# Kernel tuning notes

Hardware: AMD Instinct MI355X
Metric: run time of the kernel (lower is better)

The kernel has to match this reference:

```python
import jax, jax.numpy as jnp
import numpy as np

B, M, N = 2, 256, 256
K, P, Q, D = 8, 512, 512, 64
R, Pp, Qp, Dp = 128, 512, 512, 64
TEMP = float(np.sqrt(Dp))  # softmax temperature = sqrt(D')


def _xavier(key, shape):
    # xavier_uniform over last two dims (fan_in, fan_out), matching torch init on (K, d, D)
    fan_in, fan_out = shape[-2], shape[-1]
    lim = float(np.sqrt(6.0 / (fan_in + fan_out)))
    return jax.random.uniform(key, shape, jnp.float32, -lim, lim)


def setup_inputs() -> dict:
    key = jax.random.key(0)
    ks = jax.random.split(key, 9)
    return {
        "z": jax.random.normal(ks[0], (B, M, N, R), jnp.float32),
        "y_q": jax.random.normal(ks[1], (B, N, Qp), jnp.float32),
        "x_k": jax.random.normal(ks[2], (B, M, Pp), jnp.float32),
        "Theta_x": _xavier(ks[3], (K, P, D)),
        "Theta_y": _xavier(ks[4], (K, Q, D)),
        "Lam_x": _xavier(ks[5], (K, Pp, Dp)),
        "Lam_y": _xavier(ks[6], (K, Qp, Dp)),
        "Lam_zx": _xavier(ks[7], (K, R, Dp)),
        "Lam_zy": _xavier(ks[8], (K, R, Dp)),
    }


def reference(z, y_q, x_k, Theta_x, Theta_y, Lam_x, Lam_y, Lam_zx, Lam_zy):
    # --- mixed attention scores ---
    xt = jnp.einsum('bmp,kpd->bkmd', x_k, Lam_x)          # [B,K,M,D']
    yt = jnp.einsum('bnq,kqd->bknd', y_q, Lam_y)          # [B,K,N,D']
    r = jnp.einsum('bkmd,bknd->bkmn', xt, yt)             # pairwise term
    zy = jnp.einsum('bmnr,krd->bkmnd', z, Lam_zy)         # [B,K,M,N,D'] (large)
    r = r + jnp.einsum('bkmnd,bkmd->bkmn', zy, xt)
    r = r + jnp.einsum('bknd,bmnr,krd->bkmn', yt, z, Lam_zx)
    # --- generalised convolution (mask=None, bias=False) ---
    a = jax.nn.softmax(r / TEMP, axis=-2)                 # softmax over M (column-wise)
    xv = jnp.einsum('bmp,kpd->bkmd', x_k, Theta_x)        # value projection
    y = jnp.einsum('bkmn,bkmd,kqd->bnq', a, xv, Theta_y)  # [B,N,Q]
    return y
```

## Files before the change

kernel.cpp:

```cpp
#include <hip/hip_runtime.h>
#include <hip/hip_bf16.h>

#define LOG2E_OVER_T 0.18033688011112042f

typedef __attribute__((ext_vector_type(8))) short short8;
typedef __attribute__((ext_vector_type(4))) float f32x4;
typedef unsigned short ushort_t;
typedef unsigned long long ull_t;

#define MFMA16(a, b, c) __builtin_amdgcn_mfma_f32_16x16x32_bf16(a, b, c, 0, 0, 0)

__device__ __forceinline__ ushort_t f2bf(float f) {
    union { float f; unsigned u; } v; v.f = f;
    unsigned r = (v.u + 0x7fffu + ((v.u >> 16) & 1u)) >> 16;
    return (ushort_t)r;
}

__device__ __forceinline__ void split8(const float4 a, const float4 b,
                                       short8& hi, short8& lo)
{
    union { float f[8]; unsigned u[8]; } Z;
    Z.f[0] = a.x; Z.f[1] = a.y; Z.f[2] = a.z; Z.f[3] = a.w;
    Z.f[4] = b.x; Z.f[5] = b.y; Z.f[6] = b.z; Z.f[7] = b.w;
    union { unsigned u[4]; short8 s; } H, L;
    #pragma unroll
    for (int i = 0; i < 4; i++) {
        const unsigned u0 = Z.u[2 * i], u1 = Z.u[2 * i + 1];
        H.u[i] = __builtin_amdgcn_perm(u1, u0, 0x07060302u);
        union { unsigned u; float f; } h0, h1;
        h0.u = u0 & 0xffff0000u; h1.u = u1 & 0xffff0000u;
        union { float f; unsigned u; } l0, l1;
        l0.f = Z.f[2 * i] - h0.f; l1.f = Z.f[2 * i + 1] - h1.f;
        L.u[i] = __builtin_amdgcn_perm(l1.u, l0.u, 0x07060302u);
    }
    hi = H.s; lo = L.s;
}

__device__ __forceinline__ void mfma_core64(
    const ushort_t* __restrict__ Ag, int lda,
    const ushort_t* __restrict__ Btg, int ldb,
    int ksteps, f32x4 acc[2][2])
{
    __shared__ __align__(16) ushort_t As[64 * 40];
    __shared__ __align__(16) ushort_t Bs[64 * 40];
    const int t = threadIdx.x;
    const int srow = t >> 2, skc = (t & 3) * 8;
    const int lane = t & 63, w = t >> 6;
    const int wr = w >> 1, wc = w & 1;
    const int fr = lane & 15, kg = lane >> 4;
    const int aoff = (wr * 32 + fr) * 40 + kg * 8;
    const int boff = (wc * 32 + fr) * 40 + kg * 8;
    const long arow = (long)srow * lda + skc;
    const long brow = (long)srow * ldb + skc;

    short8 ra = *(const short8*)(Ag + arow);
    short8 rb = *(const short8*)(Btg + brow);
    for (int kt = 0; kt < ksteps; kt++) {
        __syncthreads();
        *(short8*)&As[srow * 40 + skc] = ra;
        *(short8*)&Bs[srow * 40 + skc] = rb;
        __syncthreads();
        if (kt + 1 < ksteps) {
            ra = *(const short8*)(Ag + arow + (kt + 1) * 32);
            rb = *(const short8*)(Btg + brow + (kt + 1) * 32);
        }
        short8 a0 = *(const short8*)&As[aoff];
        short8 a1 = *(const short8*)&As[aoff + 16 * 40];
        short8 b0 = *(const short8*)&Bs[boff];
        short8 b1 = *(const short8*)&Bs[boff + 16 * 40];
        acc[0][0] = MFMA16(a0, b0, acc[0][0]);
        acc[0][1] = MFMA16(a0, b1, acc[0][1]);
        acc[1][0] = MFMA16(a1, b0, acc[1][0]);
        acc[1][1] = MFMA16(a1, b1, acc[1][1]);
    }
}

__device__ __forceinline__ void zero_acc(f32x4 acc[2][2]) {
    const f32x4 z4 = {0.f, 0.f, 0.f, 0.f};
    acc[0][0] = z4; acc[0][1] = z4; acc[1][0] = z4; acc[1][1] = z4;
}

__global__ __launch_bounds__(256)
void convert_kernel(const float* __restrict__ x_k, const float* __restrict__ y_q,
                    const float* __restrict__ Lam_x, const float* __restrict__ Theta_x,
                    const float* __restrict__ Lam_y, const float* __restrict__ Lam_zy,
                    const float* __restrict__ Lam_zx, const float* __restrict__ Theta_y,
                    ushort_t* __restrict__ xkb, ushort_t* __restrict__ yqb,
                    ushort_t* __restrict__ WxTb, ushort_t* __restrict__ WyTb,
                    ushort_t* __restrict__ Zyb, ushort_t* __restrict__ Zxb,
                    ushort_t* __restrict__ TyTb, float* __restrict__ ssum)
{
    int i = blockIdx.x * 256 + threadIdx.x;
    if (i < 262144) { xkb[i] = f2bf(x_k[i]); return; }
    i -= 262144;
    if (i < 262144) { yqb[i] = f2bf(y_q[i]); return; }
    i -= 262144;
    if (i < 524288) {
        const int k = i >> 16, rem = i & 65535, dc = rem >> 9, p = i & 511;
        const float v = (dc < 64) ? Lam_x[((long)k * 512 + p) * 64 + dc]
                                  : Theta_x[((long)k * 512 + p) * 64 + dc - 64];
        WxTb[i] = f2bf(v); return;
    }
    i -= 524288;
    if (i < 262144) {
        const int k = i >> 15, d = (i >> 9) & 63, p = i & 511;
        WyTb[i] = f2bf(Lam_y[((long)k * 512 + p) * 64 + d]); return;
    }
    i -= 262144;
    if (i < 65536) { Zyb[i] = f2bf(Lam_zy[i]); return; }
    i -= 65536;
    if (i < 65536) { Zxb[i] = f2bf(Lam_zx[i]); return; }
    i -= 65536;
    if (i < 262144) {
        const int q = i >> 9, kd = i & 511, k = kd >> 6, d = kd & 63;
        TyTb[i] = f2bf(Theta_y[((long)k * 512 + q) * 64 + d]); return;
    }
    i -= 262144;
    ssum[i] = 0.f;
}

__global__ __launch_bounds__(256)
void proj_kernel(const ushort_t* __restrict__ xkb, const ushort_t* __restrict__ yqb,
                 const ushort_t* __restrict__ WxTb, const ushort_t* __restrict__ WyTb,
                 ushort_t* __restrict__ xtb, ushort_t* __restrict__ ytb,
                 ushort_t* __restrict__ xvTb)
{
    const int side = blockIdx.z;
    const int bx = blockIdx.x, by = blockIdx.y;
    if (side == 1 && bx >= 8) return;
    f32x4 acc[2][2]; zero_acc(acc);
    const int t = threadIdx.x, lane = t & 63, w = t >> 6;
    const int wr = w >> 1, wc = w & 1, fr = lane & 15, kg = lane >> 4;

    if (side == 0) {
        mfma_core64(xkb + (long)(by * 64) * 512, 512,
                    WxTb + (long)(bx * 64) * 512, 512, 16, acc);
        const int k = bx >> 1, isxv = bx & 1;
        #pragma unroll
        for (int mi = 0; mi < 2; mi++)
        #pragma unroll
        for (int ni = 0; ni < 2; ni++) {
            const int grow0 = by * 64 + wr * 32 + mi * 16 + kg * 4;
            const int b = grow0 >> 8, m0 = grow0 & 255;
            const int d = wc * 32 + ni * 16 + fr;
            if (!isxv) {
                #pragma unroll
                for (int j = 0; j < 4; j++)
                    xtb[(((long)(b * 8 + k)) * 256 + m0 + j) * 64 + d] = f2bf(acc[mi][ni][j]);
            } else {
                ull_t pk = (ull_t)f2bf(acc[mi][ni][0])
                         | ((ull_t)f2bf(acc[mi][ni][1]) << 16)
                         | ((ull_t)f2bf(acc[mi][ni][2]) << 32)
                         | ((ull_t)f2bf(acc[mi][ni][3]) << 48);
                *(ull_t*)&xvTb[(((long)(b * 8 + k)) * 64 + d) * 256 + m0] = pk;
            }
        }
    } else {
        mfma_core64(yqb + (long)(by * 64) * 512, 512,
                    WyTb + (long)(bx * 64) * 512, 512, 16, acc);
        const int k = bx;
        #pragma unroll
        for (int mi = 0; mi < 2; mi++)
        #pragma unroll
        for (int ni = 0; ni < 2; ni++)
        #pragma unroll
        for (int j = 0; j < 4; j++) {
            const int grow = by * 64 + wr * 32 + mi * 16 + kg * 4 + j;
            const int b = grow >> 8, n = grow & 255;
            const int d = wc * 32 + ni * 16 + fr;
            ytb[(((long)(b * 8 + k)) * 256 + n) * 64 + d] = f2bf(acc[mi][ni][j]);
        }
    }
}

__global__ __launch_bounds__(256)
void step2_kernel(const ushort_t* __restrict__ xtb, const ushort_t* __restrict__ ytb,
                  const ushort_t* __restrict__ Zyb, const ushort_t* __restrict__ Zxb,
                  ushort_t* __restrict__ wzyb, ushort_t* __restrict__ wzxb)
{
    const int bz = blockIdx.x;
    const int which = bz >> 7, idx = bz & 127;
    const int bk = idx >> 3, tile = idx & 7, mt = tile >> 1, nt = tile & 1;
    const int k = bk & 7;
    const ushort_t* Ag  = (which ? ytb : xtb) + ((long)bk * 256 + mt * 64) * 64;
    const ushort_t* Btg = (which ? Zxb : Zyb) + ((long)k * 128 + nt * 64) * 64;
    ushort_t* C = which ? wzxb : wzyb;
    const long coff = ((long)bk * 256 + mt * 64) * 128 + nt * 64;
    f32x4 acc[2][2]; zero_acc(acc);
    mfma_core64(Ag, 64, Btg, 64, 2, acc);
    const int t = threadIdx.x, lane = t & 63, w = t >> 6;
    const int wr = w >> 1, wc = w & 1, fr = lane & 15, kg = lane >> 4;
    #pragma unroll
    for (int mi = 0; mi < 2; mi++)
    #pragma unroll
    for (int ni = 0; ni < 2; ni++)
    #pragma unroll
    for (int j = 0; j < 4; j++)
        C[coff + (long)(wr * 32 + mi * 16 + kg * 4 + j) * 128 + wc * 32 + ni * 16 + fr]
            = f2bf(acc[mi][ni][j]);
}

__global__ __launch_bounds__(256, 4)
void fused_score(const float* __restrict__ z,
                 const ushort_t* __restrict__ xtb, const ushort_t* __restrict__ ytb,
                 const ushort_t* __restrict__ wzyb, const ushort_t* __restrict__ wzxb,
                 ushort_t* __restrict__ Et, float* __restrict__ ssum)
{
    const int nt = blockIdx.x, mt = blockIdx.y, b = blockIdx.z;
    const int m0 = mt * 8, n0 = nt * 16;
    __shared__ float sc[8 * 8 * 17];
    const int t = threadIdx.x, lane = t & 63, w = t >> 6;
    const int fr = lane & 15, kg = lane >> 4;
    const int f8 = fr & 7;

    {
        const long ybase = ((long)(b * 8) * 256 + n0 + fr) * 64 + kg * 8;
        const long xbase = ((long)(b * 8) * 256 + m0 + f8) * 64 + kg * 8;
        #pragma unroll
        for (int kk = 0; kk < 2; kk++) {
            const int k = w * 2 + kk;
            const long ko = (long)k * 256 * 64;
            f32x4 acc = {0.f, 0.f, 0.f, 0.f};
            #pragma unroll
            for (int s = 0; s < 2; s++) {
                short8 av = *(const short8*)(ytb + ybase + ko + s * 32);
                short8 bv = *(const short8*)(xtb + xbase + ko + s * 32);
                acc = MFMA16(av, bv, acc);
            }
            if (fr < 8) {
                #pragma unroll
                for (int j = 0; j < 4; j++)
                    sc[k * 136 + fr * 17 + kg * 4 + j] = acc[j];
            }
        }
    }
    __syncthreads();

    {
        #pragma unroll
        for (int mi = 0; mi < 2; mi++) {
            const int ml = w * 2 + mi;
            const int m = m0 + ml;
            const float* zr = z + (((long)b * 256 + m) * 256 + n0 + fr) * 128 + kg * 8;
            const ushort_t* wp = wzyb + (((long)b * 8 + f8) * 256 + m) * 128 + kg * 8;
            f32x4 acc = {0.f, 0.f, 0.f, 0.f};
            #pragma unroll
            for (int s = 0; s < 4; s++) {
                float4 z0 = *(const float4*)(zr + s * 32);
                float4 z1 = *(const float4*)(zr + s * 32 + 4);
                short8 wv = *(const short8*)(wp + s * 32);
                short8 hi, lo;
                split8(z0, z1, hi, lo);
                acc = MFMA16(hi, wv, acc);
                acc = MFMA16(lo, wv, acc);
            }
            if (fr < 8) {
                #pragma unroll
                for (int j = 0; j < 4; j++)
                    sc[fr * 136 + ml * 17 + kg * 4 + j] += acc[j];
            }
        }
    }
    __syncthreads();

    {
        #pragma unroll
        for (int ni = 0; ni < 4; ni++) {
            const int nl = w * 4 + ni;
            const int n = n0 + nl;
            const float* zr = z + (((long)b * 256 + m0 + f8) * 256 + n) * 128 + kg * 8;
            const ushort_t* wp = wzxb + (((long)b * 8 + f8) * 256 + n) * 128 + kg * 8;
            f32x4 acc = {0.f, 0.f, 0.f, 0.f};
            #pragma unroll
            for (int s = 0; s < 4; s++) {
                float4 z0 = *(const float4*)(zr + s * 32);
                float4 z1 = *(const float4*)(zr + s * 32 + 4);
                short8 wv = *(const short8*)(wp + s * 32);
                short8 hi, lo;
                split8(z0, z1, hi, lo);
                acc = MFMA16(hi, wv, acc);
                acc = MFMA16(lo, wv, acc);
            }
            if (fr < 8 && kg < 2) {
                #pragma unroll
                for (int j = 0; j < 4; j++)
                    sc[fr * 136 + (kg * 4 + j) * 17 + nl] += acc[j];
            }
        }
    }
    __syncthreads();

    if (t < 128) {
        const int k = t >> 4, nl = t & 15;
        float sum = 0.f;
        ushort_t eb[8];
        #pragma unroll
        for (int j = 0; j < 8; j++) {
            const float e = exp2f(sc[k * 136 + j * 17 + nl] * LOG2E_OVER_T);
            eb[j] = f2bf(e);
            sum += e;
        }
        *(short8*)(Et + (((long)b * 8 + k) * 256 + n0 + nl) * 256 + m0) = *(short8*)eb;
        atomicAdd(&ssum[(b * 8 + k) * 256 + n0 + nl], sum);
    }
}

__global__ __launch_bounds__(256)
void ogemm_kernel(const ushort_t* __restrict__ Et, const ushort_t* __restrict__ xvTb,
                  const float* __restrict__ ssum, ushort_t* __restrict__ o2b)
{
    const int mt = blockIdx.x, bk = blockIdx.y;
    f32x4 acc[2][2]; zero_acc(acc);
    mfma_core64(Et + ((long)bk * 256 + mt * 64) * 256, 256,
                xvTb + (long)bk * 64 * 256, 256, 8, acc);
    const int t = threadIdx.x, lane = t & 63, w = t >> 6;
    const int wr = w >> 1, wc = w & 1, fr = lane & 15, kg = lane >> 4;
    const int b = bk >> 3, k = bk & 7;
    #pragma unroll
    for (int mi = 0; mi < 2; mi++)
    #pragma unroll
    for (int j = 0; j < 4; j++) {
        const int n = mt * 64 + wr * 32 + mi * 16 + kg * 4 + j;
        const float inv = 1.0f / ssum[bk * 256 + n];
        #pragma unroll
        for (int ni = 0; ni < 2; ni++) {
            const int d = wc * 32 + ni * 16 + fr;
            o2b[((long)b * 256 + n) * 512 + k * 64 + d] = f2bf(acc[mi][ni][j] * inv);
        }
    }
}

__global__ __launch_bounds__(256)
void ygemm_kernel(const ushort_t* __restrict__ o2b, const ushort_t* __restrict__ TyTb,
                  float* __restrict__ out)
{
    const int qt = blockIdx.x, mt = blockIdx.y, b = blockIdx.z;
    f32x4 acc[2][2]; zero_acc(acc);
    mfma_core64(o2b + ((long)b * 256 + mt * 64) * 512, 512,
                TyTb + (long)qt * 64 * 512, 512, 16, acc);
    const int t = threadIdx.x, lane = t & 63, w = t >> 6;
    const int wr = w >> 1, wc = w & 1, fr = lane & 15, kg = lane >> 4;
    #pragma unroll
    for (int mi = 0; mi < 2; mi++)
    #pragma unroll
    for (int ni = 0; ni < 2; ni++)
    #pragma unroll
    for (int j = 0; j < 4; j++) {
        const int n = mt * 64 + wr * 32 + mi * 16 + kg * 4 + j;
        const int q = qt * 64 + wc * 32 + ni * 16 + fr;
        out[((long)b * 256 + n) * 512 + q] = acc[mi][ni][j];
    }
}

extern "C" void kernel_launch(void* const* d_in, const int* in_sizes, int n_in,
                              void* d_out, int out_size, void* d_ws, size_t ws_size,
                              hipStream_t stream)
{
    const float* z       = (const float*)d_in[0];
    const float* y_q     = (const float*)d_in[1];
    const float* x_k     = (const float*)d_in[2];
    const float* Theta_x = (const float*)d_in[3];
    const float* Theta_y = (const float*)d_in[4];
    const float* Lam_x   = (const float*)d_in[5];
    const float* Lam_y   = (const float*)d_in[6];
    const float* Lam_zx  = (const float*)d_in[7];
    const float* Lam_zy  = (const float*)d_in[8];
    float* out = (float*)d_out;

    ushort_t* U = (ushort_t*)d_ws;
    ushort_t* xkb  = U;
    ushort_t* yqb  = U + 262144;
    ushort_t* WxTb = U + 524288;
    ushort_t* WyTb = U + 1048576;
    ushort_t* Zyb  = U + 1310720;
    ushort_t* Zxb  = U + 1376256;
    ushort_t* TyTb = U + 1441792;
    ushort_t* xtb  = U + 1703936;
    ushort_t* ytb  = U + 1966080;
    ushort_t* xvTb = U + 2228224;
    ushort_t* wzyb = U + 2490368;
    ushort_t* wzxb = U + 3014656;
    ushort_t* Et   = U + 3538944;
    ushort_t* o2b  = U + 4587520;
    float*    ssum = (float*)(U + 4849664);

    convert_kernel<<<6672, 256, 0, stream>>>(x_k, y_q, Lam_x, Theta_x, Lam_y,
        Lam_zy, Lam_zx, Theta_y, xkb, yqb, WxTb, WyTb, Zyb, Zxb, TyTb, ssum);

    proj_kernel<<<dim3(16, 8, 2), 256, 0, stream>>>(xkb, yqb, WxTb, WyTb,
        xtb, ytb, xvTb);

    step2_kernel<<<256, 256, 0, stream>>>(xtb, ytb, Zyb, Zxb, wzyb, wzxb);

    fused_score<<<dim3(16, 32, 2), 256, 0, stream>>>(z, xtb, ytb, wzyb, wzxb,
        Et, ssum);

    ogemm_kernel<<<dim3(4, 16), 256, 0, stream>>>(Et, xvTb, ssum, o2b);

    ygemm_kernel<<<dim3(8, 4, 2), 256, 0, stream>>>(o2b, TyTb, out);
}
```

Baseline: 71.05 us.

## Stage z tile once in shared memory as bf16 hi/lo split for both score terms

The fused score kernel now loads each z element from global memory once per block, splits it into bf16 hi/lo halves a single time, and stores them in a swizzled shared-memory tile that both the zy and zx contractions read. Before, each z element was fetched and split twice, once per contraction. The block now covers 32 n columns in four chunks, with register prefetch of the next chunk and a double-buffered score array so the softmax-exponent epilogue of one chunk overlaps the next. The wz intermediates are stored in an m-major, k-interleaved layout to match the new access pattern. This costs about 32KB of shared memory per block, drops the occupancy hint and halves the grid, which may reduce latency hiding.

```diff
diff --git a/kernel.cpp b/kernel.cpp
--- a/kernel.cpp
+++ b/kernel.cpp
@@ -34,6 +34,10 @@
         L.u[i] = __builtin_amdgcn_perm(l1.u, l0.u, 0x07060302u);
     }
     hi = H.s; lo = L.s;
+}
+
+__device__ __forceinline__ int phys16(int c16, int key) {
+    return (c16 & 3) | ((((c16 >> 2) ^ key) & 7) << 2);
 }
 
 __device__ __forceinline__ void mfma_core64(
@@ -181,11 +185,10 @@
     const int bz = blockIdx.x;
     const int which = bz >> 7, idx = bz & 127;
     const int bk = idx >> 3, tile = idx & 7, mt = tile >> 1, nt = tile & 1;
-    const int k = bk & 7;
+    const int k = bk & 7, b = bk >> 3;
     const ushort_t* Ag  = (which ? ytb : xtb) + ((long)bk * 256 + mt * 64) * 64;
     const ushort_t* Btg = (which ? Zxb : Zyb) + ((long)k * 128 + nt * 64) * 64;
     ushort_t* C = which ? wzxb : wzyb;
-    const long coff = ((long)bk * 256 + mt * 64) * 128 + nt * 64;
     f32x4 acc[2][2]; zero_acc(acc);
     mfma_core64(Ag, 64, Btg, 64, 2, acc);
     const int t = threadIdx.x, lane = t & 63, w = t >> 6;
@@ -195,113 +198,164 @@
     #pragma unroll
     for (int ni = 0; ni < 2; ni++)
     #pragma unroll
-    for (int j = 0; j < 4; j++)
-        C[coff + (long)(wr * 32 + mi * 16 + kg * 4 + j) * 128 + wc * 32 + ni * 16 + fr]
-            = f2bf(acc[mi][ni][j]);
-}
-
-__global__ __launch_bounds__(256, 4)
+    for (int j = 0; j < 4; j++) {
+        const int m_glob = mt * 64 + wr * 32 + mi * 16 + kg * 4 + j;
+        const int r_glob = nt * 64 + wc * 32 + ni * 16 + fr;
+        C[(((long)b * 256 + m_glob) * 8 + k) * 128 + r_glob] = f2bf(acc[mi][ni][j]);
+    }
+}
+
+__global__ __launch_bounds__(256)
 void fused_score(const float* __restrict__ z,
                  const ushort_t* __restrict__ xtb, const ushort_t* __restrict__ ytb,
                  const ushort_t* __restrict__ wzyb, const ushort_t* __restrict__ wzxb,
                  ushort_t* __restrict__ Et, float* __restrict__ ssum)
 {
-    const int nt = blockIdx.x, mt = blockIdx.y, b = blockIdx.z;
-    const int m0 = mt * 8, n0 = nt * 16;
-    __shared__ float sc[8 * 8 * 17];
-    const int t = threadIdx.x, lane = t & 63, w = t >> 6;
+    const int ns = blockIdx.x;
+    const int mt = blockIdx.y;
+    const int b  = blockIdx.z;
+    const int m0 = mt * 8;
+    const int nbase = ns * 32;
+
+    __shared__ __align__(16) ushort_t zhl[64 * 256];
+    __shared__ float sc[2][8][8][9];
+    __shared__ float t1[8][8][34];
+
+    const int tid = threadIdx.x;
+    const int lane = tid & 63, w = tid >> 6;
     const int fr = lane & 15, kg = lane >> 4;
     const int f8 = fr & 7;
 
-    {
-        const long ybase = ((long)(b * 8) * 256 + n0 + fr) * 64 + kg * 8;
-        const long xbase = ((long)(b * 8) * 256 + m0 + f8) * 64 + kg * 8;
-        #pragma unroll
-        for (int kk = 0; kk < 2; kk++) {
-            const int k = w * 2 + kk;
-            const long ko = (long)k * 256 * 64;
+    const int r_id = tid >> 2;
+    const int zm = r_id >> 3, zn = r_id & 7;
+    const int skey = zn ^ zm;
+    const float* zrow_base = z + (((long)b * 256 + m0 + zm) * 256 + nbase + zn) * 128
+                               + (tid & 3) * 32;
+    float4 zr[8];
+    #pragma unroll
+    for (int i = 0; i < 8; i++) zr[i] = *(const float4*)(zrow_base + i * 4);
+
+    #pragma unroll
+    for (int kk = 0; kk < 2; kk++) {
+        const int k = w * 2 + kk;
+        const long kb = (long)(b * 8 + k) * 256;
+        #pragma unroll
+        for (int nsub = 0; nsub < 2; nsub++) {
             f32x4 acc = {0.f, 0.f, 0.f, 0.f};
             #pragma unroll
             for (int s = 0; s < 2; s++) {
-                short8 av = *(const short8*)(ytb + ybase + ko + s * 32);
-                short8 bv = *(const short8*)(xtb + xbase + ko + s * 32);
+                short8 av = *(const short8*)(ytb + (kb + nbase + nsub * 16 + fr) * 64 + kg * 8 + s * 32);
+                short8 bv = *(const short8*)(xtb + (kb + m0 + f8) * 64 + kg * 8 + s * 32);
                 acc = MFMA16(av, bv, acc);
             }
             if (fr < 8) {
                 #pragma unroll
                 for (int j = 0; j < 4; j++)
-                    sc[k * 136 + fr * 17 + kg * 4 + j] = acc[j];
+                    t1[k][fr][nsub * 16 + kg * 4 + j] = acc[j];
             }
         }
     }
     __syncthreads();
 
-    {
+    for (int c = 0; c < 4; c++) {
+        #pragma unroll
+        for (int i = 0; i < 4; i++) {
+            const int u = (i + (tid & 3)) & 3;
+            short8 hi, lo;
+            split8(zr[2 * u], zr[2 * u + 1], hi, lo);
+            const int c16h = (tid & 3) * 4 + u;
+            *(short8*)&zhl[r_id * 256 + phys16(c16h, skey) * 8] = hi;
+            *(short8*)&zhl[r_id * 256 + phys16(c16h + 16, skey) * 8] = lo;
+        }
+        if (c < 3) {
+            #pragma unroll
+            for (int i = 0; i < 8; i++)
+                zr[i] = *(const float4*)(zrow_base + (c + 1) * 1024 + i * 4);
+        }
+        __syncthreads();
+
         #pragma unroll
         for (int mi = 0; mi < 2; mi++) {
-            const int ml = w * 2 + mi;
-            const int m = m0 + ml;
-            const float* zr = z + (((long)b * 256 + m) * 256 + n0 + fr) * 128 + kg * 8;
-            const ushort_t* wp = wzyb + (((long)b * 8 + f8) * 256 + m) * 128 + kg * 8;
+            const int m_loc = w * 2 + mi;
+            const int keyr = f8 ^ m_loc;
+            const int rowb = (m_loc * 8 + f8) * 256;
+            const ushort_t* wp = wzyb + (((long)b * 256 + m0 + m_loc) * 8 + f8) * 128 + kg * 8;
+            short8 wb[4], ah[4], al[4];
+            #pragma unroll
+            for (int s = 0; s < 4; s++) wb[s] = *(const short8*)(wp + s * 32);
+            #pragma unroll
+            for (int s = 0; s < 4; s++) {
+                ah[s] = *(const short8*)&zhl[rowb + phys16(kg + 4 * s, keyr) * 8];
+                al[s] = *(const short8*)&zhl[rowb + phys16(16 + kg + 4 * s, keyr) * 8];
+            }
             f32x4 acc = {0.f, 0.f, 0.f, 0.f};
             #pragma unroll
-            for (int s = 0; s < 4; s++) {
-                float4 z0 = *(const float4*)(zr + s * 32);
-                float4 z1 = *(const float4*)(zr + s * 32 + 4);
-                short8 wv = *(const short8*)(wp + s * 32);
-                short8 hi, lo;
-                split8(z0, z1, hi, lo);
-                acc = MFMA16(hi, wv, acc);
-                acc = MFMA16(lo, wv, acc);
-            }
-            if (fr < 8) {
-                #pragma unroll
-                for (int j = 0; j < 4; j++)
-                    sc[fr * 136 + ml * 17 + kg * 4 + j] += acc[j];
-            }
-        }
-    }
-    __syncthreads();
-
-    {
-        #pragma unroll
-        for (int ni = 0; ni < 4; ni++) {
-            const int nl = w * 4 + ni;
-            const int n = n0 + nl;
-            const float* zr = z + (((long)b * 256 + m0 + f8) * 256 + n) * 128 + kg * 8;
-            const ushort_t* wp = wzxb + (((long)b * 8 + f8) * 256 + n) * 128 + kg * 8;
-            f32x4 acc = {0.f, 0.f, 0.f, 0.f};
-            #pragma unroll
-            for (int s = 0; s < 4; s++) {
-                float4 z0 = *(const float4*)(zr + s * 32);
-                float4 z1 = *(const float4*)(zr + s * 32 + 4);
-                short8 wv = *(const short8*)(wp + s * 32);
-                short8 hi, lo;
-                split8(z0, z1, hi, lo);
-                acc = MFMA16(hi, wv, acc);
-                acc = MFMA16(lo, wv, acc);
-            }
+            for (int s = 0; s < 4; s++) acc = MFMA16(ah[s], wb[s], acc);
+            #pragma unroll
+            for (int s = 0; s < 4; s++) acc = MFMA16(al[s], wb[s], acc);
             if (fr < 8 && kg < 2) {
                 #pragma unroll
                 for (int j = 0; j < 4; j++)
-                    sc[fr * 136 + (kg * 4 + j) * 17 + nl] += acc[j];
-            }
-        }
-    }
-    __syncthreads();
-
-    if (t < 128) {
-        const int k = t >> 4, nl = t & 15;
-        float sum = 0.f;
-        ushort_t eb[8];
-        #pragma unroll
-        for (int j = 0; j < 8; j++) {
-            const float e = exp2f(sc[k * 136 + j * 17 + nl] * LOG2E_OVER_T);
-            eb[j] = f2bf(e);
-            sum += e;
-        }
-        *(short8*)(Et + (((long)b * 8 + k) * 256 + n0 + nl) * 256 + m0) = *(short8*)eb;
-        atomicAdd(&ssum[(b * 8 + k) * 256 + n0 + nl], sum);
+                    sc[c & 1][m_loc][fr][kg * 4 + j] = acc[j];
+            }
+        }
+        __syncthreads();
+
+        #pragma unroll
+        for (int ni = 0; ni < 2; ni++) {
+            const int n_loc = w * 2 + ni;
+            const int keyr = n_loc ^ f8;
+            const int rowb = (f8 * 8 + n_loc) * 256;
+            const ushort_t* wp = wzxb + (((long)b * 256 + nbase + c * 8 + n_loc) * 8 + f8) * 128 + kg * 8;
+            short8 wb[4], ah[4], al[4];
+            #pragma unroll
+            for (int s = 0; s < 4; s++) wb[s] = *(const short8*)(wp + s * 32);
+            #pragma unroll
+            for (int s = 0; s < 4; s++) {
+                ah[s] = *(const short8*)&zhl[rowb + phys16(kg + 4 * s, keyr) * 8];
+                al[s] = *(const short8*)&zhl[rowb + phys16(16 + kg + 4 * s, keyr) * 8];
+            }
+            f32x4 acc = {0.f, 0.f, 0.f, 0.f};
+            #pragma unroll
+            for (int s = 0; s < 4; s++) acc = MFMA16(ah[s], wb[s], acc);
+            #pragma unroll
+            for (int s = 0; s < 4; s++) acc = MFMA16(al[s], wb[s], acc);
+            if (fr < 8 && kg < 2) {
+                #pragma unroll
+                for (int j = 0; j < 4; j++)
+                    sc[c & 1][kg * 4 + j][fr][n_loc] += acc[j];
+            }
+        }
+
+        if (c > 0 && lane < 16) {
+            const int cp = c - 1;
+            const int k = w * 2 + (lane >> 3);
+            const int nl = lane & 7;
+            const int nloc = cp * 8 + nl;
+            float s8 = 0.f; ushort_t eb[8];
+            #pragma unroll
+            for (int m = 0; m < 8; m++) {
+                const float e = exp2f((sc[cp & 1][m][k][nl] + t1[k][m][nloc]) * LOG2E_OVER_T);
+                eb[m] = f2bf(e); s8 += e;
+            }
+            *(short8*)(Et + (((long)b * 8 + k) * 256 + nbase + nloc) * 256 + m0) = *(short8*)eb;
+            atomicAdd(&ssum[(b * 8 + k) * 256 + nbase + nloc], s8);
+        }
+        __syncthreads();
+    }
+
+    if (lane < 16) {
+        const int k = w * 2 + (lane >> 3);
+        const int nl = lane & 7;
+        const int nloc = 3 * 8 + nl;
+        float s8 = 0.f; ushort_t eb[8];
+        #pragma unroll
+        for (int m = 0; m < 8; m++) {
+            const float e = exp2f((sc[1][m][k][nl] + t1[k][m][nloc]) * LOG2E_OVER_T);
+            eb[m] = f2bf(e); s8 += e;
+        }
+        *(short8*)(Et + (((long)b * 8 + k) * 256 + nbase + nloc) * 256 + m0) = *(short8*)eb;
+        atomicAdd(&ssum[(b * 8 + k) * 256 + nbase + nloc], s8);
     }
 }
 
@@ -392,7 +446,7 @@
 
     step2_kernel<<<256, 256, 0, stream>>>(xtb, ytb, Zyb, Zxb, wzyb, wzxb);
 
-    fused_score<<<dim3(16, 32, 2), 256, 0, stream>>>(z, xtb, ytb, wzyb, wzxb,
+    fused_score<<<dim3(8, 32, 2), 256, 0, stream>>>(z, xtb, ytb, wzyb, wzxb,
         Et, ssum);
 
     ogemm_kernel<<<dim3(4, 16), 256, 0, stream>>>(Et, xvTb, ssum, o2b);
```

Result: slower. 78.83 us (+11.0%).

## Split fused_score reduction dimension across two waves and relayout wz intermediates

Applied to the files above, without the earlier changes.

The fused score kernel now runs with 128 threads. Each of its two waves handles one half of the R=128 reduction dimension, and the partial sums go into separate shared-memory buffers, which lets the kernel drop the intermediate __syncthreads barriers. The step2 output layout changes to [b][m][k][r] so the wz weight loads for all 8 heads of one m or n are contiguous. The pairwise xt·yt term is computed by wave 0 alone. In exchange, each thread does more serial work and each block has fewer threads, which could reduce latency hiding.

```diff
diff --git a/kernel.cpp b/kernel.cpp
--- a/kernel.cpp
+++ b/kernel.cpp
@@ -181,11 +181,10 @@
     const int bz = blockIdx.x;
     const int which = bz >> 7, idx = bz & 127;
     const int bk = idx >> 3, tile = idx & 7, mt = tile >> 1, nt = tile & 1;
-    const int k = bk & 7;
+    const int k = bk & 7, b = bk >> 3;
     const ushort_t* Ag  = (which ? ytb : xtb) + ((long)bk * 256 + mt * 64) * 64;
     const ushort_t* Btg = (which ? Zxb : Zyb) + ((long)k * 128 + nt * 64) * 64;
     ushort_t* C = which ? wzxb : wzyb;
-    const long coff = ((long)bk * 256 + mt * 64) * 128 + nt * 64;
     f32x4 acc[2][2]; zero_acc(acc);
     mfma_core64(Ag, 64, Btg, 64, 2, acc);
     const int t = threadIdx.x, lane = t & 63, w = t >> 6;
@@ -195,113 +194,117 @@
     #pragma unroll
     for (int ni = 0; ni < 2; ni++)
     #pragma unroll
-    for (int j = 0; j < 4; j++)
-        C[coff + (long)(wr * 32 + mi * 16 + kg * 4 + j) * 128 + wc * 32 + ni * 16 + fr]
-            = f2bf(acc[mi][ni][j]);
-}
-
-__global__ __launch_bounds__(256, 4)
+    for (int j = 0; j < 4; j++) {
+        const int m_glob = mt * 64 + wr * 32 + mi * 16 + kg * 4 + j;
+        const int r_glob = nt * 64 + wc * 32 + ni * 16 + fr;
+        C[(((long)b * 256 + m_glob) * 8 + k) * 128 + r_glob] = f2bf(acc[mi][ni][j]);
+    }
+}
+
+__global__ __launch_bounds__(128)
 void fused_score(const float* __restrict__ z,
                  const ushort_t* __restrict__ xtb, const ushort_t* __restrict__ ytb,
                  const ushort_t* __restrict__ wzyb, const ushort_t* __restrict__ wzxb,
                  ushort_t* __restrict__ Et, float* __restrict__ ssum)
 {
     const int nt = blockIdx.x, mt = blockIdx.y, b = blockIdx.z;
-    const int m0 = mt * 8, n0 = nt * 16;
-    __shared__ float sc[8 * 8 * 17];
-    const int t = threadIdx.x, lane = t & 63, w = t >> 6;
+    const int nbase = nt * 16, m0 = mt * 8;
+    __shared__ float sc[2][8][8][17];
+
+    const int tid = threadIdx.x;
+    const int lane = tid & 63, w = tid >> 6;
     const int fr = lane & 15, kg = lane >> 4;
     const int f8 = fr & 7;
-
-    {
-        const long ybase = ((long)(b * 8) * 256 + n0 + fr) * 64 + kg * 8;
-        const long xbase = ((long)(b * 8) * 256 + m0 + f8) * 64 + kg * 8;
-        #pragma unroll
-        for (int kk = 0; kk < 2; kk++) {
-            const int k = w * 2 + kk;
-            const long ko = (long)k * 256 * 64;
+    const int rh = w * 64;
+
+    if (w == 0) {
+        #pragma unroll 2
+        for (int k = 0; k < 8; k++) {
+            const long kb = (long)(b * 8 + k) * 256;
+            short8 a0 = *(const short8*)(ytb + (kb + nbase + fr) * 64 + kg * 8);
+            short8 b0 = *(const short8*)(xtb + (kb + m0 + f8) * 64 + kg * 8);
+            short8 a1 = *(const short8*)(ytb + (kb + nbase + fr) * 64 + 32 + kg * 8);
+            short8 b1 = *(const short8*)(xtb + (kb + m0 + f8) * 64 + 32 + kg * 8);
             f32x4 acc = {0.f, 0.f, 0.f, 0.f};
-            #pragma unroll
-            for (int s = 0; s < 2; s++) {
-                short8 av = *(const short8*)(ytb + ybase + ko + s * 32);
-                short8 bv = *(const short8*)(xtb + xbase + ko + s * 32);
-                acc = MFMA16(av, bv, acc);
-            }
+            acc = MFMA16(a0, b0, acc);
+            acc = MFMA16(a1, b1, acc);
             if (fr < 8) {
                 #pragma unroll
                 for (int j = 0; j < 4; j++)
-                    sc[k * 136 + fr * 17 + kg * 4 + j] = acc[j];
+                    sc[0][fr][k][kg * 4 + j] = acc[j];
             }
         }
     }
-    __syncthreads();
-
-    {
-        #pragma unroll
-        for (int mi = 0; mi < 2; mi++) {
-            const int ml = w * 2 + mi;
-            const int m = m0 + ml;
-            const float* zr = z + (((long)b * 256 + m) * 256 + n0 + fr) * 128 + kg * 8;
-            const ushort_t* wp = wzyb + (((long)b * 8 + f8) * 256 + m) * 128 + kg * 8;
-            f32x4 acc = {0.f, 0.f, 0.f, 0.f};
-            #pragma unroll
-            for (int s = 0; s < 4; s++) {
-                float4 z0 = *(const float4*)(zr + s * 32);
-                float4 z1 = *(const float4*)(zr + s * 32 + 4);
-                short8 wv = *(const short8*)(wp + s * 32);
-                short8 hi, lo;
-                split8(z0, z1, hi, lo);
-                acc = MFMA16(hi, wv, acc);
-                acc = MFMA16(lo, wv, acc);
-            }
-            if (fr < 8) {
+
+    #pragma unroll 2
+    for (int m = 0; m < 8; m++) {
+        const float* zp = z + (((long)b * 256 + m0 + m) * 256 + nbase + fr) * 128 + rh + kg * 8;
+        const ushort_t* wp = wzyb + (((long)b * 256 + m0 + m) * 8 + f8) * 128 + rh + kg * 8;
+        const float4 z00 = *(const float4*)(zp);
+        const float4 z01 = *(const float4*)(zp + 4);
+        const float4 z10 = *(const float4*)(zp + 32);
+        const float4 z11 = *(const float4*)(zp + 36);
+        const short8 w0 = *(const short8*)(wp);
+        const short8 w1 = *(const short8*)(wp + 32);
+        short8 h0, l0, h1, l1;
+        split8(z00, z01, h0, l0);
+        split8(z10, z11, h1, l1);
+        f32x4 acc = {0.f, 0.f, 0.f, 0.f};
+        acc = MFMA16(h0, w0, acc);
+        acc = MFMA16(h1, w1, acc);
+        acc = MFMA16(l0, w0, acc);
+        acc = MFMA16(l1, w1, acc);
+        if (fr < 8) {
+            if (w == 0) {
                 #pragma unroll
                 for (int j = 0; j < 4; j++)
-                    sc[fr * 136 + ml * 17 + kg * 4 + j] += acc[j];
-            }
-        }
-    }
-    __syncthreads();
-
-    {
-        #pragma unroll
-        for (int ni = 0; ni < 4; ni++) {
-            const int nl = w * 4 + ni;
-            const int n = n0 + nl;
-            const float* zr = z + (((long)b * 256 + m0 + f8) * 256 + n) * 128 + kg * 8;
-            const ushort_t* wp = wzxb + (((long)b * 8 + f8) * 256 + n) * 128 + kg * 8;
-            f32x4 acc = {0.f, 0.f, 0.f, 0.f};
-            #pragma unroll
-            for (int s = 0; s < 4; s++) {
-                float4 z0 = *(const float4*)(zr + s * 32);
-                float4 z1 = *(const float4*)(zr + s * 32 + 4);
-                short8 wv = *(const short8*)(wp + s * 32);
-                short8 hi, lo;
-                split8(z0, z1, hi, lo);
-                acc = MFMA16(hi, wv, acc);
-                acc = MFMA16(lo, wv, acc);
-            }
-            if (fr < 8 && kg < 2) {
+                    sc[0][m][fr][kg * 4 + j] += acc[j];
+            } else {
                 #pragma unroll
                 for (int j = 0; j < 4; j++)
-                    sc[fr * 136 + (kg * 4 + j) * 17 + nl] += acc[j];
+                    sc[1][m][fr][kg * 4 + j] = acc[j];
             }
         }
     }
+
+    #pragma unroll 2
+    for (int n = 0; n < 16; n++) {
+        const float* zp = z + (((long)b * 256 + m0 + f8) * 256 + nbase + n) * 128 + rh + kg * 8;
+        const ushort_t* wp = wzxb + (((long)b * 256 + nbase + n) * 8 + f8) * 128 + rh + kg * 8;
+        const float4 z00 = *(const float4*)(zp);
+        const float4 z01 = *(const float4*)(zp + 4);
+        const float4 z10 = *(const float4*)(zp + 32);
+        const float4 z11 = *(const float4*)(zp + 36);
+        const short8 w0 = *(const short8*)(wp);
+        const short8 w1 = *(const short8*)(wp + 32);
+        short8 h0, l0, h1, l1;
+        split8(z00, z01, h0, l0);
+        split8(z10, z11, h1, l1);
+        f32x4 acc = {0.f, 0.f, 0.f, 0.f};
+        acc = MFMA16(h0, w0, acc);
+        acc = MFMA16(h1, w1, acc);
+        acc = MFMA16(l0, w0, acc);
+        acc = MFMA16(l1, w1, acc);
+        if (fr < 8 && kg < 2) {
+            #pragma unroll
+            for (int j = 0; j < 4; j++)
+                sc[w][kg * 4 + j][fr][n] += acc[j];
+        }
+    }
     __syncthreads();
 
-    if (t < 128) {
-        const int k = t >> 4, nl = t & 15;
-        float sum = 0.f;
+    {
+        const int k = tid >> 4, n = tid & 15;
+        float s8 = 0.f;
         ushort_t eb[8];
         #pragma unroll
-        for (int j = 0; j < 8; j++) {
-            const float e = exp2f(sc[k * 136 + j * 17 + nl] * LOG2E_OVER_T);
-            eb[j] = f2bf(e);
-            sum += e;
-        }
-        *(short8*)(Et + (((long)b * 8 + k) * 256 + n0 + nl) * 256 + m0) = *(short8*)eb;
-        atomicAdd(&ssum[(b * 8 + k) * 256 + n0 + nl], sum);
+        for (int m = 0; m < 8; m++) {
+            const float e = exp2f((sc[0][m][k][n] + sc[1][m][k][n]) * LOG2E_OVER_T);
+            eb[m] = f2bf(e);
+            s8 += e;
+        }
+        *(short8*)(Et + (((long)b * 8 + k) * 256 + nbase + n) * 256 + m0) = *(short8*)eb;
+        atomicAdd(&ssum[(b * 8 + k) * 256 + nbase + n], s8);
     }
 }
 
@@ -392,7 +395,7 @@
 
     step2_kernel<<<256, 256, 0, stream>>>(xtb, ytb, Zyb, Zxb, wzyb, wzxb);
 
-    fused_score<<<dim3(16, 32, 2), 256, 0, stream>>>(z, xtb, ytb, wzyb, wzxb,
+    fused_score<<<dim3(16, 32, 2), 128, 0, stream>>>(z, xtb, ytb, wzyb, wzxb,
         Et, ssum);
 
     ogemm_kernel<<<dim3(4, 16), 256, 0, stream>>>(Et, xvTb, ssum, o2b);
```

Measured after the change: 71.26 us. No clear change (+0.3%).
